# Kernel tuning notes

Measured on AMD Instinct MI355X. Metric: run time of the kernel, lower is better.

## Reference

```python
import jax, jax.numpy as jnp
import numpy as np
from jax import lax

B, N, S, K = 16, 4096, 1024, 32
C_PTS = 64
MLP = [64, 64, 128]
BN_EPS = 1e-5


def _fps(xyz, npoint):
    """Farthest point sampling. xyz: [B,N,3] -> idx [B,npoint] int32."""
    b, n, _ = xyz.shape
    def body(carry, _):
        dist, farthest = carry                       # [B,N], [B]
        centroid = xyz[jnp.arange(b), farthest]      # [B,3]
        d = jnp.sum((xyz - centroid[:, None, :]) ** 2, axis=-1)  # [B,N]
        dist = jnp.minimum(dist, d)
        nxt = jnp.argmax(dist, axis=-1).astype(jnp.int32)
        return (dist, nxt), farthest
    init = (jnp.full((b, n), 1e10, dtype=xyz.dtype), jnp.zeros((b,), jnp.int32))
    _, idxs = lax.scan(body, init, None, length=npoint)  # [npoint, B]
    return idxs.T


def _gather(pts, idx):
    """pts: [B,N,C], idx: [B,S,K] -> [B,S,K,C] (per-batch gather)."""
    return jax.vmap(lambda p, i: p[i])(pts, idx)


def setup_inputs() -> dict:
    key = jax.random.key(0)
    ks = jax.random.split(key, 16)
    inp = {
        "xyz": jax.random.normal(ks[0], (B, N, 3), jnp.float32),
        "points": jax.random.normal(ks[1], (B, N, C_PTS), jnp.float32),
    }
    last = 3 + C_PTS
    ki = 2
    for i, out_c in enumerate(MLP):
        scale = 1.0 / np.sqrt(last)
        inp[f"w{i}"] = jax.random.normal(ks[ki], (last, out_c), jnp.float32) * scale
        inp[f"b{i}"] = jnp.zeros((out_c,), jnp.float32)
        inp[f"g{i}"] = jnp.ones((out_c,), jnp.float32)
        inp[f"be{i}"] = jnp.zeros((out_c,), jnp.float32)
        last = out_c
        ki += 1
    return inp


def _forward(xyz, points, params):
    fps_idx = _fps(xyz, S)                                    # [B,S]
    new_xyz = jnp.take_along_axis(xyz, fps_idx[..., None], axis=1)  # [B,S,3]
    # KNN: pairwise squared distances centroids -> all points
    d = (jnp.sum(new_xyz ** 2, -1)[:, :, None]
         - 2.0 * jnp.einsum('bsc,bnc->bsn', new_xyz, xyz)
         + jnp.sum(xyz ** 2, -1)[:, None, :])                 # [B,S,N]
    _, knn_idx = lax.top_k(-d, K)                             # [B,S,K]
    grouped_xyz = _gather(xyz, knn_idx) - new_xyz[:, :, None, :]   # [B,S,K,3]
    grouped_pts = _gather(points, knn_idx)                    # [B,S,K,C]
    x = jnp.concatenate([grouped_xyz, grouped_pts], axis=-1)  # [B,S,K,3+C]
    for (w, b, g, be) in params:
        x = jnp.einsum('bskc,cd->bskd', x, w) + b             # 1x1 conv
        mean = jnp.mean(x, axis=(0, 1, 2))                    # BN (train stats)
        var = jnp.var(x, axis=(0, 1, 2))
        x = (x - mean) * lax.rsqrt(var + BN_EPS) * g + be
        x = jax.nn.relu(x)
    new_points = jnp.max(x, axis=2)                           # max over nsample
    return new_xyz, new_points


def reference(xyz, points, w0, b0, g0, be0, w1, b1, g1, be1, w2, b2, g2, be2):
    params = [(w0, b0, g0, be0), (w1, b1, g1, be1), (w2, b2, g2, be2)]
    return _forward(xyz, points, params)
```

## Files before the change

### kernel.cpp

```cpp
#include <hip/hip_runtime.h>
#include <float.h>
#include <math.h>

#define B_ 16
#define N_ 4096
#define S_ 1024
#define K_ 32
#define CIN0 67
#define NBS (B_ * S_)
#define NEWXYZ_FLOATS (B_ * S_ * 3)
#define AST 68
#define AQ (K_ * AST)
#define QB 4


__device__ __forceinline__ float sqdist3(float x, float y, float z,
                                         float cx, float cy, float cz) {
#pragma clang fp contract(off)
  float dx = x - cx, dy = y - cy, dz = z - cz;
  float s = dx * dx;
  s = s + dy * dy;
  s = s + dz * dz;
  return s;
}

__device__ __forceinline__ float knn_dist(float c2, float cx, float cy, float cz,
                                          float x, float y, float z) {
#pragma clang fp contract(off)
  float dot = cx * x; dot = dot + cy * y; dot = dot + cz * z;
  float x2 = x * x;   x2 = x2 + y * y;   x2 = x2 + z * z;
  float d = c2 - 2.0f * dot;
  d = d + x2;
  return d;
}

template <int CTRL>
__device__ __forceinline__ float dpp_f(float v, float oldv) {
  return __int_as_float(__builtin_amdgcn_update_dpp(
      __float_as_int(oldv), __float_as_int(v), CTRL, 0xF, 0xF, false));
}
template <int CTRL>
__device__ __forceinline__ int dpp_i(int v, int oldv) {
  return __builtin_amdgcn_update_dpp(oldv, v, CTRL, 0xF, 0xF, false);
}

template <int CTRL>
__device__ __forceinline__ void fps_combine2(float& val, int& idx) {
  const float tv = dpp_f<CTRL>(val, -1.0f);
  const int ti = dpp_i<CTRL>(idx, 0x7fffffff);
  const bool take = (tv > val) || (tv == val && ti < idx);
  val = take ? tv : val;
  idx = take ? ti : idx;
}

__global__ __launch_bounds__(256, 1) void fps_kernel(
    const float* __restrict__ xyz, float* __restrict__ newxyz) {
  const int b = blockIdx.x;
  const int t = threadIdx.x;
  __shared__ float4 sp[N_];
  __shared__ float2 rec[2][4];
  __shared__ float cbuf[S_ * 3];
  const float* xb = xyz + (size_t)b * N_ * 3;
  for (int p = t; p < N_; p += 256) {
    sp[p] = make_float4(xb[p * 3 + 0], xb[p * 3 + 1], xb[p * 3 + 2], 0.0f);
  }
  float ax[16], ay[16], az[16];
#pragma unroll
  for (int j = 0; j < 16; ++j) {
    const int p = t * 16 + j;
    const float x = xb[p * 3 + 0];
    const float y = xb[p * 3 + 1];
    const float z = xb[p * 3 + 2];
    asm volatile("v_accvgpr_write_b32 %0, %1" : "=a"(ax[j]) : "v"(x));
    asm volatile("v_accvgpr_write_b32 %0, %1" : "=a"(ay[j]) : "v"(y));
    asm volatile("v_accvgpr_write_b32 %0, %1" : "=a"(az[j]) : "v"(z));
  }
  float dist[16];
#pragma unroll
  for (int j = 0; j < 16; ++j) dist[j] = 1e10f;
  __syncthreads();
  float cx = xb[0], cy = xb[1], cz = xb[2];
  for (int s = 0; s < S_; ++s) {
    if (t == 0) {
      cbuf[s * 3 + 0] = cx;
      cbuf[s * 3 + 1] = cy;
      cbuf[s * 3 + 2] = cz;
    }
    float dd[16];
#pragma unroll
    for (int j = 0; j < 16; ++j) {
      float x, y, z;
      asm volatile("v_accvgpr_read_b32 %0, %1" : "=v"(x) : "a"(ax[j]));
      asm volatile("v_accvgpr_read_b32 %0, %1" : "=v"(y) : "a"(ay[j]));
      asm volatile("v_accvgpr_read_b32 %0, %1" : "=v"(z) : "a"(az[j]));
      dd[j] = sqdist3(x, y, z, cx, cy, cz);
    }
    __builtin_amdgcn_sched_barrier(0);
    float best = -1.0f;
    int bi = 0;
#pragma unroll
    for (int j = 0; j < 16; ++j) {
      const float nd = fminf(dist[j], dd[j]);
      dist[j] = nd;
      const bool take = nd > best;
      best = take ? nd : best;
      bi = take ? (t * 16 + j) : bi;
    }
    fps_combine2<0x111>(best, bi);
    fps_combine2<0x112>(best, bi);
    fps_combine2<0x114>(best, bi);
    fps_combine2<0x118>(best, bi);
    fps_combine2<0x142>(best, bi);
    fps_combine2<0x143>(best, bi);
    const float wv = __int_as_float(__builtin_amdgcn_readlane(__float_as_int(best), 63));
    const int wi = __builtin_amdgcn_readlane(bi, 63);
    const int par = s & 1;
    if ((t & 63) == 0) {
      rec[par][t >> 6] = make_float2(wv, __int_as_float(wi));
    }
    __syncthreads();
    float2 r0 = rec[par][0];
    float bv = r0.x;
    int bj = __float_as_int(r0.y);
#pragma unroll
    for (int w = 1; w < 4; ++w) {
      const float2 r = rec[par][w];
      const int iw = __float_as_int(r.y);
      const bool take = (r.x > bv) || (r.x == bv && iw < bj);
      bv = take ? r.x : bv;
      bj = take ? iw : bj;
    }
    const float4 c = sp[bj];
    cx = c.x; cy = c.y; cz = c.z;
  }
  __syncthreads();
  float* ob = newxyz + (size_t)b * S_ * 3;
  for (int i = t; i < S_ * 3; i += 256) ob[i] = cbuf[i];
}

__global__ __launch_bounds__(256, 2) void knn_kernel(
    const float* __restrict__ xyz, const float* __restrict__ newxyz,
    int* __restrict__ knn_idx) {
  const int bs0 = blockIdx.x * 4;
  const int b = bs0 >> 10;
  const int t = threadIdx.x;
  const int wave = t >> 6;
  const int lane = t & 63;
  __shared__ float sxx[N_];
  __shared__ float sxy[N_];
  __shared__ float sxz[N_];
  const float* xb = xyz + (size_t)b * N_ * 3;
  for (int p = t; p < N_; p += 256) {
    sxx[p] = xb[p * 3 + 0];
    sxy[p] = xb[p * 3 + 1];
    sxz[p] = xb[p * 3 + 2];
  }
  __syncthreads();
  const int bs = bs0 + wave;
  const float cx = newxyz[(size_t)bs * 3 + 0];
  const float cy = newxyz[(size_t)bs * 3 + 1];
  const float cz = newxyz[(size_t)bs * 3 + 2];
  float c2;
  {
#pragma clang fp contract(off)
    float s = cx * cx;
    s = s + cy * cy;
    s = s + cz * cz;
    c2 = s;
  }
  float d[64];
  float gval[8];
  int gidx[8];
#pragma unroll
  for (int g = 0; g < 8; ++g) {
    float gv = FLT_MAX;
    int gi = g * 8;
#pragma unroll
    for (int q = 0; q < 8; ++q) {
      const int j = g * 8 + q;
      const int p = j * 64 + lane;
      const float dd = knn_dist(c2, cx, cy, cz, sxx[p], sxy[p], sxz[p]);
      d[j] = dd;
      if (dd < gv) { gv = dd; gi = j; }
    }
    gval[g] = gv; gidx[g] = gi;
  }
  int* krow = knn_idx + (size_t)bs * K_;
  for (int it = 0; it < K_; ++it) {
    float best = gval[0];
    int bj = gidx[0];
#pragma unroll
    for (int g = 1; g < 8; ++g) {
      if (gval[g] < best || (gval[g] == best && gidx[g] < bj)) { best = gval[g]; bj = gidx[g]; }
    }
    int bidx = bj * 64 + lane;
#pragma unroll
    for (int off = 32; off >= 1; off >>= 1) {
      const float ov = __shfl_xor(best, off);
      const int oi = __shfl_xor(bidx, off);
      if (ov < best || (ov == best && oi < bidx)) { best = ov; bidx = oi; }
    }
    if (lane == 0) krow[it] = bidx;
    if (lane == (bidx & 63)) {
      const int jl = bidx >> 6;
      const int gg = jl >> 3;
      const int qq = jl & 7;
#pragma unroll
      for (int g = 0; g < 8; ++g) {
        if (g == gg) {
#pragma unroll
          for (int q = 0; q < 8; ++q) {
            d[g * 8 + q] = (q == qq) ? FLT_MAX : d[g * 8 + q];
          }
          float gv = FLT_MAX;
          int gi = g * 8;
#pragma unroll
          for (int q = 0; q < 8; ++q) {
            const int j = g * 8 + q;
            if (d[j] < gv) { gv = d[j]; gi = j; }
          }
          gval[g] = gv; gidx[g] = gi;
        }
      }
    }
  }
}


__device__ __forceinline__ void loadw0p(float* __restrict__ wbuf,
                                        const float* __restrict__ w0, int t) {
  for (int i = t; i < 68 * 64; i += 256) {
    const int c = i >> 6;
    wbuf[i] = (c < 67) ? w0[i] : 0.0f;
  }
}
__device__ __forceinline__ void loadw64(float* __restrict__ wbuf,
                                        const float* __restrict__ w, int t) {
  for (int i = t; i < 64 * 64; i += 256) wbuf[i] = w[i];
}
__device__ __forceinline__ void loadw_half(float* __restrict__ wbuf,
                                           const float* __restrict__ w2, int ofs, int t) {
  for (int i = t; i < 64 * 64; i += 256) {
    const int c = i >> 6, j = i & 63;
    wbuf[i] = w2[c * 128 + ofs + j];
  }
}

__device__ __forceinline__ void build4(float* __restrict__ act,
    const float* __restrict__ xyz, const float* __restrict__ points,
    const int* __restrict__ knn_idx, const float* __restrict__ newxyz,
    int bs0, int t) {
  const int b = bs0 >> 10;
  for (int i = t; i < QB * K_ * AST; i += 256) {
    const int q = i / AQ;
    const int rem = i - q * AQ;
    const int k = rem / AST;
    const int c = rem - k * AST;
    const int bs = bs0 + q;
    const int p = knn_idx[(size_t)bs * K_ + k];
    float v;
    if (c < 3) {
      v = xyz[((size_t)b * N_ + p) * 3 + c] - newxyz[(size_t)bs * 3 + c];
    } else if (c < 67) {
      v = points[((size_t)b * N_ + p) * 64 + (c - 3)];
    } else {
      v = 0.0f;
    }
    act[i] = v;
  }
}

template <int CQ>
__device__ __forceinline__ void mm4(const float* __restrict__ actq,
    const float* __restrict__ wbuf, const float* __restrict__ bias,
    float acc[4][8], int kslot, int g) {
#pragma unroll
  for (int j = 0; j < 8; ++j) {
    const float bj = bias[g * 8 + j];
#pragma unroll
    for (int i = 0; i < 4; ++i) acc[i][j] = bj;
  }
  for (int qd = 0; qd < CQ; ++qd) {
    float4 a[4];
#pragma unroll
    for (int i = 0; i < 4; ++i)
      a[i] = *(const float4*)&actq[(kslot * 4 + i) * AST + qd * 4];
#pragma unroll
    for (int cc = 0; cc < 4; ++cc) {
      const float4 wlo = *(const float4*)&wbuf[(qd * 4 + cc) * 64 + g * 8];
      const float4 whi = *(const float4*)&wbuf[(qd * 4 + cc) * 64 + g * 8 + 4];
#pragma unroll
      for (int i = 0; i < 4; ++i) {
        const float x = (cc == 0) ? a[i].x : (cc == 1) ? a[i].y
                        : (cc == 2) ? a[i].z : a[i].w;
        acc[i][0] += x * wlo.x;
        acc[i][1] += x * wlo.y;
        acc[i][2] += x * wlo.z;
        acc[i][3] += x * wlo.w;
        acc[i][4] += x * whi.x;
        acc[i][5] += x * whi.y;
        acc[i][6] += x * whi.z;
        acc[i][7] += x * whi.w;
      }
    }
  }
}

__device__ __forceinline__ void stats4(const float acc[4][8],
    float* __restrict__ psum, float* __restrict__ psq, int bs, int ofs, int r) {
  float s[8], ss[8];
#pragma unroll
  for (int j = 0; j < 8; ++j) {
    s[j] = ((acc[0][j] + acc[1][j]) + acc[2][j]) + acc[3][j];
    ss[j] = ((acc[0][j] * acc[0][j] + acc[1][j] * acc[1][j]) +
             acc[2][j] * acc[2][j]) + acc[3][j] * acc[3][j];
  }
#pragma unroll
  for (int m = 8; m <= 32; m <<= 1) {
#pragma unroll
    for (int j = 0; j < 8; ++j) {
      s[j] += __shfl_xor(s[j], m);
      ss[j] += __shfl_xor(ss[j], m);
    }
  }
  if (r < 8) {
#pragma unroll
    for (int j = 0; j < 8; ++j) {
      psum[(size_t)bs * 128 + ofs + r * 8 + j] = s[j];
      psq[(size_t)bs * 128 + ofs + r * 8 + j] = ss[j];
    }
  }
}

__device__ __forceinline__ void minmax4(const float acc[4][8],
    float* __restrict__ maxraw, float* __restrict__ minbuf, int bs, int ofs, int r) {
  float mx[8], mn[8];
#pragma unroll
  for (int j = 0; j < 8; ++j) {
    mx[j] = fmaxf(fmaxf(acc[0][j], acc[1][j]), fmaxf(acc[2][j], acc[3][j]));
    mn[j] = fminf(fminf(acc[0][j], acc[1][j]), fminf(acc[2][j], acc[3][j]));
  }
#pragma unroll
  for (int m = 8; m <= 32; m <<= 1) {
#pragma unroll
    for (int j = 0; j < 8; ++j) {
      mx[j] = fmaxf(mx[j], __shfl_xor(mx[j], m));
      mn[j] = fminf(mn[j], __shfl_xor(mn[j], m));
    }
  }
  if (r < 8) {
#pragma unroll
    for (int j = 0; j < 8; ++j) {
      maxraw[(size_t)bs * 128 + ofs + r * 8 + j] = mx[j];
      minbuf[(size_t)bs * 128 + ofs + r * 8 + j] = mn[j];
    }
  }
}

__device__ __forceinline__ void zstore4(const float acc[4][8],
    float* __restrict__ zrow, int kslot, int g) {
#pragma unroll
  for (int i = 0; i < 4; ++i) {
    const int base = (kslot * 4 + i) * 64 + g * 8;
    *(float4*)&zrow[base] = make_float4(acc[i][0], acc[i][1], acc[i][2], acc[i][3]);
    *(float4*)&zrow[base + 4] = make_float4(acc[i][4], acc[i][5], acc[i][6], acc[i][7]);
  }
}


__global__ __launch_bounds__(256, 2) void passA4_kernel(
    const float* __restrict__ xyz, const float* __restrict__ points,
    const float* __restrict__ newxyz, const int* __restrict__ knn_idx,
    const float* __restrict__ w0, const float* __restrict__ b0,
    float* __restrict__ psum, float* __restrict__ psq, float* __restrict__ zbuf) {
  __shared__ __align__(16) float act[QB * AQ];
  __shared__ __align__(16) float wbuf[68 * 64];
  const int bs0 = blockIdx.x * QB, t = threadIdx.x;
  build4(act, xyz, points, knn_idx, newxyz, bs0, t);
  loadw0p(wbuf, w0, t);
  __syncthreads();
  const int q = t >> 6, r = t & 63, ks = r >> 3, g = r & 7;
  float acc[4][8];
  mm4<17>(act + q * AQ, wbuf, b0, acc, ks, g);
  stats4(acc, psum, psq, bs0 + q, 0, r);
  zstore4(acc, zbuf + (size_t)(bs0 + q) * 2048, ks, g);
}

__global__ __launch_bounds__(256, 2) void passB4_kernel(
    const float* __restrict__ w1, const float* __restrict__ b1,
    const float* __restrict__ scales, const float* __restrict__ shifts,
    float* __restrict__ psum, float* __restrict__ psq, float* __restrict__ zbuf) {
  __shared__ __align__(16) float act[QB * AQ];
  __shared__ __align__(16) float wbuf[64 * 64];
  const int bs0 = blockIdx.x * QB, t = threadIdx.x;
  const float* zb = zbuf + (size_t)bs0 * 2048;
  for (int i = t; i < QB * 2048; i += 256) {
    const int q2 = i >> 11;
    const int rem = i & 2047;
    const int k = rem >> 6;
    const int c = rem & 63;
    const float v = zb[i] * scales[c] + shifts[c];
    act[q2 * AQ + k * AST + c] = fmaxf(v, 0.0f);
  }
  loadw64(wbuf, w1, t);
  __syncthreads();
  const int q = t >> 6, r = t & 63, ks = r >> 3, g = r & 7;
  float acc[4][8];
  mm4<16>(act + q * AQ, wbuf, b1, acc, ks, g);
  stats4(acc, psum, psq, bs0 + q, 0, r);
  zstore4(acc, zbuf + (size_t)(bs0 + q) * 2048, ks, g);
}

__global__ __launch_bounds__(256, 2) void passC4_kernel(
    const float* __restrict__ w2, const float* __restrict__ b2,
    const float* __restrict__ scales1, const float* __restrict__ shifts1,
    float* __restrict__ psum, float* __restrict__ psq,
    float* __restrict__ maxraw, float* __restrict__ minbuf,
    const float* __restrict__ zbuf) {
  __shared__ __align__(16) float act[QB * AQ];
  __shared__ __align__(16) float wbuf[64 * 64];
  const int bs0 = blockIdx.x * QB, t = threadIdx.x;
  const float* zb = zbuf + (size_t)bs0 * 2048;
  for (int i = t; i < QB * 2048; i += 256) {
    const int q2 = i >> 11;
    const int rem = i & 2047;
    const int k = rem >> 6;
    const int c = rem & 63;
    const float v = zb[i] * scales1[c] + shifts1[c];
    act[q2 * AQ + k * AST + c] = fmaxf(v, 0.0f);
  }
  loadw_half(wbuf, w2, 0, t);
  __syncthreads();
  const int q = t >> 6, r = t & 63, ks = r >> 3, g = r & 7;
  float acc[4][8];
  mm4<16>(act + q * AQ, wbuf, b2, acc, ks, g);
  stats4(acc, psum, psq, bs0 + q, 0, r);
  minmax4(acc, maxraw, minbuf, bs0 + q, 0, r);
  __syncthreads();
  loadw_half(wbuf, w2, 64, t);
  __syncthreads();
  mm4<16>(act + q * AQ, wbuf, b2 + 64, acc, ks, g);
  stats4(acc, psum, psq, bs0 + q, 64, r);
  minmax4(acc, maxraw, minbuf, bs0 + q, 64, r);
}


__device__ __forceinline__ void loadw(float* __restrict__ wbuf,
                                      const float* __restrict__ w, int n, int t) {
  for (int i = t; i < n; i += 256) wbuf[i] = w[i];
}

__device__ __forceinline__ void build_x0(float* __restrict__ act,
    const float* __restrict__ xyz, const float* __restrict__ points,
    const int* __restrict__ knn_idx, const float* __restrict__ newxyz,
    int bs, int t) {
  const int b = bs >> 10;
  const int* krow = knn_idx + (size_t)bs * K_;
  const float cx = newxyz[(size_t)bs * 3 + 0];
  const float cy = newxyz[(size_t)bs * 3 + 1];
  const float cz = newxyz[(size_t)bs * 3 + 2];
  for (int i = t; i < K_ * CIN0; i += 256) {
    const int k = i / CIN0;
    const int c = i - k * CIN0;
    const int p = krow[k];
    float v;
    if (c < 3) {
      v = xyz[((size_t)b * N_ + p) * 3 + c] - (c == 0 ? cx : (c == 1 ? cy : cz));
    } else {
      v = points[((size_t)b * N_ + p) * 64 + (c - 3)];
    }
    act[k * AST + c] = v;
  }
}

template <int CIN>
__device__ __forceinline__ void matmul64(const float* __restrict__ act,
    const float* __restrict__ wbuf, const float* __restrict__ bias,
    float* __restrict__ out, int t) {
  const int k = t >> 3;
  const int g = t & 7;
  float acc[8];
#pragma unroll
  for (int j = 0; j < 8; ++j) acc[j] = bias[g * 8 + j];
  for (int c = 0; c < CIN; ++c) {
    const float xv = act[k * AST + c];
    const float4 wa = *(const float4*)&wbuf[c * 64 + g * 8];
    const float4 wb = *(const float4*)&wbuf[c * 64 + g * 8 + 4];
    acc[0] += xv * wa.x; acc[1] += xv * wa.y;
    acc[2] += xv * wa.z; acc[3] += xv * wa.w;
    acc[4] += xv * wb.x; acc[5] += xv * wb.y;
    acc[6] += xv * wb.z; acc[7] += xv * wb.w;
  }
  *(float4*)&out[k * AST + g * 8] = make_float4(acc[0], acc[1], acc[2], acc[3]);
  *(float4*)&out[k * AST + g * 8 + 4] = make_float4(acc[4], acc[5], acc[6], acc[7]);
}

__device__ __forceinline__ void norm_relu64(float* __restrict__ act,
    const float* __restrict__ scale, const float* __restrict__ shift, int t) {
  for (int i = t; i < K_ * 64; i += 256) {
    const int k = i >> 6, c = i & 63;
    const float v = act[k * AST + c] * scale[c] + shift[c];
    act[k * AST + c] = fmaxf(v, 0.0f);
  }
}

__device__ __forceinline__ void stats64(const float* __restrict__ out,
    float* __restrict__ psum, float* __restrict__ psq, int bs, int ofs, int t) {
  if (t < 64) {
    float s = 0.f, q = 0.f;
    for (int k = 0; k < K_; ++k) {
      const float v = out[k * AST + t];
      s += v; q += v * v;
    }
    psum[(size_t)bs * 128 + ofs + t] = s;
    psq[(size_t)bs * 128 + ofs + t] = q;
  }
}

__device__ __forceinline__ void minmax64(const float* __restrict__ out,
    float* __restrict__ maxraw, float* __restrict__ minbuf, int bs, int ofs, int t) {
  if (t >= 64 && t < 128) {
    const int ch = t - 64;
    float mx = -FLT_MAX, mn = FLT_MAX;
    for (int k = 0; k < K_; ++k) {
      const float v = out[k * AST + ch];
      mx = fmaxf(mx, v); mn = fminf(mn, v);
    }
    maxraw[(size_t)bs * 128 + ofs + ch] = mx;
    minbuf[(size_t)bs * 128 + ofs + ch] = mn;
  }
}

__global__ __launch_bounds__(256) void passA_kernel(
    const float* __restrict__ xyz, const float* __restrict__ points,
    const float* __restrict__ newxyz, const int* __restrict__ knn_idx,
    const float* __restrict__ w0, const float* __restrict__ b0,
    float* __restrict__ psum, float* __restrict__ psq) {
  __shared__ __align__(16) float actA[K_ * AST];
  __shared__ __align__(16) float outB[K_ * AST];
  __shared__ __align__(16) float wbuf[CIN0 * 64];
  const int bs = blockIdx.x, t = threadIdx.x;
  build_x0(actA, xyz, points, knn_idx, newxyz, bs, t);
  loadw(wbuf, w0, CIN0 * 64, t);
  __syncthreads();
  matmul64<CIN0>(actA, wbuf, b0, outB, t);
  __syncthreads();
  stats64(outB, psum, psq, bs, 0, t);
}

__global__ __launch_bounds__(256) void passB_kernel(
    const float* __restrict__ xyz, const float* __restrict__ points,
    const float* __restrict__ newxyz, const int* __restrict__ knn_idx,
    const float* __restrict__ w0, const float* __restrict__ b0,
    const float* __restrict__ w1, const float* __restrict__ b1,
    const float* __restrict__ scales, const float* __restrict__ shifts,
    float* __restrict__ psum, float* __restrict__ psq) {
  __shared__ __align__(16) float actA[K_ * AST];
  __shared__ __align__(16) float outB[K_ * AST];
  __shared__ __align__(16) float wbuf[CIN0 * 64];
  const int bs = blockIdx.x, t = threadIdx.x;
  build_x0(actA, xyz, points, knn_idx, newxyz, bs, t);
  loadw(wbuf, w0, CIN0 * 64, t);
  __syncthreads();
  matmul64<CIN0>(actA, wbuf, b0, outB, t);
  __syncthreads();
  norm_relu64(outB, scales, shifts, t);
  loadw(wbuf, w1, 64 * 64, t);
  __syncthreads();
  matmul64<64>(outB, wbuf, b1, actA, t);
  __syncthreads();
  stats64(actA, psum, psq, bs, 0, t);
}

__global__ __launch_bounds__(256) void passC_kernel(
    const float* __restrict__ xyz, const float* __restrict__ points,
    const float* __restrict__ newxyz, const int* __restrict__ knn_idx,
    const float* __restrict__ w0, const float* __restrict__ b0,
    const float* __restrict__ w1, const float* __restrict__ b1,
    const float* __restrict__ w2, const float* __restrict__ b2,
    const float* __restrict__ scales, const float* __restrict__ shifts,
    float* __restrict__ psum, float* __restrict__ psq,
    float* __restrict__ maxraw, float* __restrict__ minbuf) {
  __shared__ __align__(16) float actA[K_ * AST];
  __shared__ __align__(16) float outB[K_ * AST];
  __shared__ __align__(16) float wbuf[CIN0 * 64];
  const int bs = blockIdx.x, t = threadIdx.x;
  build_x0(actA, xyz, points, knn_idx, newxyz, bs, t);
  loadw(wbuf, w0, CIN0 * 64, t);
  __syncthreads();
  matmul64<CIN0>(actA, wbuf, b0, outB, t);
  __syncthreads();
  norm_relu64(outB, scales, shifts, t);
  loadw(wbuf, w1, 64 * 64, t);
  __syncthreads();
  matmul64<64>(outB, wbuf, b1, actA, t);
  __syncthreads();
  norm_relu64(actA, scales + 128, shifts + 128, t);
  loadw_half(wbuf, w2, 0, t);
  __syncthreads();
  matmul64<64>(actA, wbuf, b2, outB, t);
  __syncthreads();
  stats64(outB, psum, psq, bs, 0, t);
  minmax64(outB, maxraw, minbuf, bs, 0, t);
  loadw_half(wbuf, w2, 64, t);
  __syncthreads();
  matmul64<64>(actA, wbuf, b2 + 64, outB, t);
  __syncthreads();
  stats64(outB, psum, psq, bs, 64, t);
  minmax64(outB, maxraw, minbuf, bs, 64, t);
}

__global__ __launch_bounds__(256) void finalize_kernel(
    const float* __restrict__ psum, const float* __restrict__ psq,
    const float* __restrict__ g, const float* __restrict__ be,
    float* __restrict__ scale, float* __restrict__ shift) {
  const int ch = blockIdx.x, t = threadIdx.x;
  __shared__ float ss[256];
  __shared__ float sq[256];
  float s = 0.f, q = 0.f;
  for (int p = t; p < NBS; p += 256) {
    s += psum[(size_t)p * 128 + ch];
    q += psq[(size_t)p * 128 + ch];
  }
  ss[t] = s; sq[t] = q;
  __syncthreads();
  for (int off = 128; off >= 1; off >>= 1) {
    if (t < off) { ss[t] += ss[t + off]; sq[t] += sq[t + off]; }
    __syncthreads();
  }
  if (t == 0) {
    const float invN = 1.0f / (float)(B_ * S_ * K_);
    const float mean = ss[0] * invN;
    const float var = sq[0] * invN - mean * mean;
    const float sc = g[ch] / sqrtf(var + 1e-5f);
    scale[ch] = sc;
    shift[ch] = be[ch] - mean * sc;
  }
}

__global__ __launch_bounds__(256) void final_kernel(
    const float* __restrict__ minbuf, const float* __restrict__ scale,
    const float* __restrict__ shift, float* __restrict__ out) {
  const int i = blockIdx.x * 256 + threadIdx.x;
  const int ch = i & 127;
  const float sc = scale[ch], sh = shift[ch];
  const float mx = out[NEWXYZ_FLOATS + i];
  const float mn = minbuf[i];
  const float v = sc * (sc >= 0.f ? mx : mn) + sh;
  out[NEWXYZ_FLOATS + i] = fmaxf(v, 0.f);
}

extern "C" void kernel_launch(void* const* d_in, const int* in_sizes, int n_in,
                              void* d_out, int out_size, void* d_ws, size_t ws_size,
                              hipStream_t stream) {
  const float* xyz = (const float*)d_in[0];
  const float* points = (const float*)d_in[1];
  const float* w0 = (const float*)d_in[2];
  const float* b0 = (const float*)d_in[3];
  const float* g0 = (const float*)d_in[4];
  const float* be0 = (const float*)d_in[5];
  const float* w1 = (const float*)d_in[6];
  const float* b1 = (const float*)d_in[7];
  const float* g1 = (const float*)d_in[8];
  const float* be1 = (const float*)d_in[9];
  const float* w2 = (const float*)d_in[10];
  const float* b2 = (const float*)d_in[11];
  const float* g2 = (const float*)d_in[12];
  const float* be2 = (const float*)d_in[13];
  float* out = (float*)d_out;
  float* newxyz = out;
  float* maxraw = out + NEWXYZ_FLOATS;

  float* ws = (float*)d_ws;
  const size_t NEED_FAST =
      (size_t)(524288 + 16384 * 2048 + 2 * NBS * 128 + 768 + NBS * 128) * 4;

  fps_kernel<<<B_, 256, 0, stream>>>(xyz, newxyz);

  if (ws_size >= NEED_FAST) {
    int* knn_idx = (int*)ws;
    float* zbuf = ws + 524288;
    float* psum = zbuf + (size_t)16384 * 2048;
    float* psq = psum + (size_t)NBS * 128;
    float* scales = psq + (size_t)NBS * 128;
    float* shifts = scales + 384;
    float* minbuf = shifts + 384;
    knn_kernel<<<NBS / 4, 256, 0, stream>>>(xyz, newxyz, knn_idx);
    passA4_kernel<<<NBS / QB, 256, 0, stream>>>(xyz, points, newxyz, knn_idx, w0, b0,
                                                psum, psq, zbuf);
    finalize_kernel<<<64, 256, 0, stream>>>(psum, psq, g0, be0, scales, shifts);
    passB4_kernel<<<NBS / QB, 256, 0, stream>>>(w1, b1, scales, shifts, psum, psq, zbuf);
    finalize_kernel<<<64, 256, 0, stream>>>(psum, psq, g1, be1, scales + 128, shifts + 128);
    passC4_kernel<<<NBS / QB, 256, 0, stream>>>(w2, b2, scales + 128, shifts + 128,
                                                psum, psq, maxraw, minbuf, zbuf);
    finalize_kernel<<<128, 256, 0, stream>>>(psum, psq, g2, be2, scales + 256, shifts + 256);
    final_kernel<<<(B_ * S_ * 128) / 256, 256, 0, stream>>>(minbuf, scales + 256,
                                                            shifts + 256, out);
  } else {
    int* knn_idx = (int*)ws;
    float* psum = ws + 524288;
    float* psq = psum + (size_t)NBS * 128;
    float* scales = psq + (size_t)NBS * 128;
    float* shifts = scales + 384;
    float* minbuf = shifts + 384;
    knn_kernel<<<NBS / 4, 256, 0, stream>>>(xyz, newxyz, knn_idx);
    passA_kernel<<<NBS, 256, 0, stream>>>(xyz, points, newxyz, knn_idx, w0, b0, psum, psq);
    finalize_kernel<<<64, 256, 0, stream>>>(psum, psq, g0, be0, scales, shifts);
    passB_kernel<<<NBS, 256, 0, stream>>>(xyz, points, newxyz, knn_idx, w0, b0, w1, b1,
                                          scales, shifts, psum, psq);
    finalize_kernel<<<64, 256, 0, stream>>>(psum, psq, g1, be1, scales + 128, shifts + 128);
    passC_kernel<<<NBS, 256, 0, stream>>>(xyz, points, newxyz, knn_idx, w0, b0, w1, b1, w2, b2,
                                          scales, shifts, psum, psq, maxraw, minbuf);
    finalize_kernel<<<128, 256, 0, stream>>>(psum, psq, g2, be2, scales + 256, shifts + 256);
    final_kernel<<<(B_ * S_ * 128) / 256, 256, 0, stream>>>(minbuf, scales + 256,
                                                            shifts + 256, out);
  }
}
```

Measured before the change: 1.866 ms.

## Split farthest point sampling across two blocks per batch with global atomic handshake

FPS now runs two workgroups per batch, each owning half the points (8 per thread instead of 16). Each iteration the two blocks exchange their local argmax through agent-scope atomic stores and spin-loads on a tagged 64-bit slot in workspace. This halves the per-block distance work and doubles the CUs used, at the cost of a cross-CU global-memory round trip every iteration and a dependence on both blocks being co-resident. A memset of the handshake buffer is added and the workspace offsets shift to make room.

```diff
diff --git a/kernel.cpp b/kernel.cpp
--- a/kernel.cpp
+++ b/kernel.cpp
@@ -54,8 +54,10 @@
 }
 
 __global__ __launch_bounds__(256, 1) void fps_kernel(
-    const float* __restrict__ xyz, float* __restrict__ newxyz) {
-  const int b = blockIdx.x;
+    const float* __restrict__ xyz, float* __restrict__ newxyz,
+    unsigned long long* __restrict__ gbuf) {
+  const int b = blockIdx.x >> 1;
+  const int h = blockIdx.x & 1;
   const int t = threadIdx.x;
   __shared__ float4 sp[N_];
   __shared__ float2 rec[2][4];
@@ -64,10 +66,11 @@
   for (int p = t; p < N_; p += 256) {
     sp[p] = make_float4(xb[p * 3 + 0], xb[p * 3 + 1], xb[p * 3 + 2], 0.0f);
   }
-  float ax[16], ay[16], az[16];
-#pragma unroll
-  for (int j = 0; j < 16; ++j) {
-    const int p = t * 16 + j;
+  const int base = h * 2048 + t * 8;
+  float ax[8], ay[8], az[8];
+#pragma unroll
+  for (int j = 0; j < 8; ++j) {
+    const int p = base + j;
     const float x = xb[p * 3 + 0];
     const float y = xb[p * 3 + 1];
     const float z = xb[p * 3 + 2];
@@ -75,20 +78,22 @@
     asm volatile("v_accvgpr_write_b32 %0, %1" : "=a"(ay[j]) : "v"(y));
     asm volatile("v_accvgpr_write_b32 %0, %1" : "=a"(az[j]) : "v"(z));
   }
-  float dist[16];
-#pragma unroll
-  for (int j = 0; j < 16; ++j) dist[j] = 1e10f;
+  float dist[8];
+#pragma unroll
+  for (int j = 0; j < 8; ++j) dist[j] = 1e10f;
   __syncthreads();
   float cx = xb[0], cy = xb[1], cz = xb[2];
+  unsigned long long* myslots = &gbuf[(b * 2 + h) * 2];
+  unsigned long long* pslots = &gbuf[(b * 2 + (1 - h)) * 2];
   for (int s = 0; s < S_; ++s) {
-    if (t == 0) {
+    if (h == 0 && t == 0) {
       cbuf[s * 3 + 0] = cx;
       cbuf[s * 3 + 1] = cy;
       cbuf[s * 3 + 2] = cz;
     }
-    float dd[16];
-#pragma unroll
-    for (int j = 0; j < 16; ++j) {
+    float dd[8];
+#pragma unroll
+    for (int j = 0; j < 8; ++j) {
       float x, y, z;
       asm volatile("v_accvgpr_read_b32 %0, %1" : "=v"(x) : "a"(ax[j]));
       asm volatile("v_accvgpr_read_b32 %0, %1" : "=v"(y) : "a"(ay[j]));
@@ -99,12 +104,12 @@
     float best = -1.0f;
     int bi = 0;
 #pragma unroll
-    for (int j = 0; j < 16; ++j) {
+    for (int j = 0; j < 8; ++j) {
       const float nd = fminf(dist[j], dd[j]);
       dist[j] = nd;
       const bool take = nd > best;
       best = take ? nd : best;
-      bi = take ? (t * 16 + j) : bi;
+      bi = take ? (base + j) : bi;
     }
     fps_combine2<0x111>(best, bi);
     fps_combine2<0x112>(best, bi);
@@ -130,12 +135,31 @@
       bv = take ? r.x : bv;
       bj = take ? iw : bj;
     }
+    const unsigned tag = (unsigned)(s + 1);
+    if (t == 0) {
+      const unsigned long long myrec =
+          ((unsigned long long)__float_as_uint(bv) << 32) |
+          (unsigned long long)(((unsigned)bj << 11) | tag);
+      __hip_atomic_store(&myslots[par], myrec, __ATOMIC_RELEASE,
+                         __HIP_MEMORY_SCOPE_AGENT);
+    }
+    unsigned long long pr;
+    do {
+      pr = __hip_atomic_load(&pslots[par], __ATOMIC_ACQUIRE,
+                             __HIP_MEMORY_SCOPE_AGENT);
+    } while ((unsigned)(pr & 2047u) != tag);
+    const float pv = __uint_as_float((unsigned)(pr >> 32));
+    const int pj = (int)(((unsigned)pr & 0xFFFFFFFFu) >> 11);
+    const bool takeP = (pv > bv) || (pv == bv && pj < bj);
+    bj = takeP ? pj : bj;
     const float4 c = sp[bj];
     cx = c.x; cy = c.y; cz = c.z;
   }
-  __syncthreads();
-  float* ob = newxyz + (size_t)b * S_ * 3;
-  for (int i = t; i < S_ * 3; i += 256) ob[i] = cbuf[i];
+  if (h == 0) {
+    __syncthreads();
+    float* ob = newxyz + (size_t)b * S_ * 3;
+    for (int i = t; i < S_ * 3; i += 256) ob[i] = cbuf[i];
+  }
 }
 
 __global__ __launch_bounds__(256, 2) void knn_kernel(
@@ -672,14 +696,16 @@
   float* maxraw = out + NEWXYZ_FLOATS;
 
   float* ws = (float*)d_ws;
+  unsigned long long* gbuf = (unsigned long long*)ws;
   const size_t NEED_FAST =
-      (size_t)(524288 + 16384 * 2048 + 2 * NBS * 128 + 768 + NBS * 128) * 4;
-
-  fps_kernel<<<B_, 256, 0, stream>>>(xyz, newxyz);
+      (size_t)(128 + 524288 + 16384 * 2048 + 2 * NBS * 128 + 768 + NBS * 128) * 4;
+
+  hipMemsetAsync(gbuf, 0, 64 * sizeof(unsigned long long), stream);
+  fps_kernel<<<B_ * 2, 256, 0, stream>>>(xyz, newxyz, gbuf);
 
   if (ws_size >= NEED_FAST) {
-    int* knn_idx = (int*)ws;
-    float* zbuf = ws + 524288;
+    int* knn_idx = (int*)(ws + 128);
+    float* zbuf = ws + 128 + 524288;
     float* psum = zbuf + (size_t)16384 * 2048;
     float* psq = psum + (size_t)NBS * 128;
     float* scales = psq + (size_t)NBS * 128;
@@ -697,8 +723,8 @@
     final_kernel<<<(B_ * S_ * 128) / 256, 256, 0, stream>>>(minbuf, scales + 256,
                                                             shifts + 256, out);
   } else {
-    int* knn_idx = (int*)ws;
-    float* psum = ws + 524288;
+    int* knn_idx = (int*)(ws + 128);
+    float* psum = ws + 128 + 524288;
     float* psq = psum + (size_t)NBS * 128;
     float* scales = psq + (size_t)NBS * 128;
     float* shifts = scales + 384;
```

Result: slower. 3.140 ms (+68.3%).
